# Performance work log

Hardware: AMD Instinct MI355X
Metric: run time of the kernel (lower is better)

The kernel has to match this reference:

```python
import jax, jax.numpy as jnp
import numpy as np

EMBED_DIM = 512
NUM_HEADS = 16
WIN = (8, 8)
N_TOK = WIN[0] * WIN[1]           # 64 tokens per window
HEAD_DIM = EMBED_DIM // NUM_HEADS  # 32
SCALE = HEAD_DIM ** -0.5
B_WIN = 1024                       # batch * num_windows
NUM_WINDOWS = 256                  # windows per image -> batch images = 4


def _relative_bias_index(window_size):
    wh, ww = window_size
    coords = np.stack(np.meshgrid(np.arange(wh), np.arange(ww), indexing='ij'))  # (2, wh, ww)
    flat = coords.reshape(2, -1)                                   # (2, N)
    rel = (flat[:, :, None] - flat[:, None, :]).transpose(1, 2, 0)  # (N, N, 2)
    rel[:, :, 0] += wh - 1
    rel[:, :, 1] += ww - 1
    rel[:, :, 0] *= 2 * ww - 1
    return rel.sum(-1)  # (N, N) int


def setup_inputs() -> dict:
    key = jax.random.key(0)
    ks = jax.random.split(key, 6)
    x = jax.random.normal(ks[0], (B_WIN, N_TOK, EMBED_DIM), dtype=jnp.float32)
    attention_mask = jax.random.normal(ks[1], (NUM_WINDOWS, N_TOK, N_TOK), dtype=jnp.float32)
    qkv_w = jax.random.normal(ks[2], (EMBED_DIM, 3 * EMBED_DIM), dtype=jnp.float32) * 0.02
    qkv_b = jnp.zeros((3 * EMBED_DIM,), dtype=jnp.float32)
    proj_w = jax.random.normal(ks[3], (EMBED_DIM, EMBED_DIM), dtype=jnp.float32) * 0.02
    proj_b = jnp.zeros((EMBED_DIM,), dtype=jnp.float32)
    n_bias = (2 * WIN[0] - 1) * (2 * WIN[1] - 1)  # 225
    bias_table = jax.random.normal(ks[4], (n_bias, NUM_HEADS), dtype=jnp.float32) * 0.02
    rel_index = jnp.asarray(_relative_bias_index(WIN), dtype=jnp.int32)  # (N, N)
    return {"x": x, "attention_mask": attention_mask, "qkv_w": qkv_w, "qkv_b": qkv_b,
            "proj_w": proj_w, "proj_b": proj_b, "bias_table": bias_table, "rel_index": rel_index}


def reference(x, attention_mask, qkv_w, qkv_b, proj_w, proj_b, bias_table, rel_index):
    B, N, C = x.shape
    nw = attention_mask.shape[0]
    bimg = B // nw
    qkv = x @ qkv_w + qkv_b                              # (B, N, 3C)
    # original rearrange 'b n (h d c) -> d b n h c' groups last dim as (heads, 3, head_dim)
    qkv = qkv.reshape(B, N, NUM_HEADS, 3, HEAD_DIM)
    q, k, v = qkv[..., 0, :], qkv[..., 1, :], qkv[..., 2, :]  # each (B, N, H, hd)
    attn = jnp.einsum('bqhd,bkhd->bhqk', q, k) * SCALE        # (B, H, N, N)
    bias = bias_table[rel_index].transpose(2, 0, 1)           # (H, N, N)
    attn = attn + bias[None]
    attn = attn.reshape(bimg, nw, NUM_HEADS, N, N) + attention_mask[None, :, None]
    attn = jax.nn.softmax(attn, axis=-1).reshape(B, NUM_HEADS, N, N)
    out = jnp.einsum('bhqk,bkhd->bqhd', attn, v).reshape(B, N, C)
    return out @ proj_w + proj_b
```

## Files before the change

### kernel.cpp

```cpp
#include <hip/hip_runtime.h>
#include <hip/hip_bf16.h>


typedef unsigned short u16;
typedef __bf16 bx8 __attribute__((ext_vector_type(8)));
typedef float f4_t __attribute__((ext_vector_type(4)));

#define QKV_ELEMS 33554432ull
#define SCALE 0.17677669529663687f

static __device__ __forceinline__ u16 f2b(float f) {
    return __builtin_bit_cast(u16, (__bf16)f);
}

typedef const unsigned int __attribute__((address_space(1)))* gas_t;
typedef unsigned int __attribute__((address_space(3)))* las_t;
static __device__ __forceinline__ void glds16(const void* g, void* l) {
    __builtin_amdgcn_global_load_lds((gas_t)g, (las_t)l, 16, 0, 0);
}

__global__ void cvt_k(const float* __restrict__ X, u16* __restrict__ Xb) {
    size_t i = ((size_t)blockIdx.x * 256 + threadIdx.x) * 8;
    float4 v0 = *(const float4*)(X + i);
    float4 v1 = *(const float4*)(X + i + 4);
    ushort4 p0, p1;
    p0.x = f2b(v0.x); p0.y = f2b(v0.y); p0.z = f2b(v0.z); p0.w = f2b(v0.w);
    p1.x = f2b(v1.x); p1.y = f2b(v1.y); p1.z = f2b(v1.z); p1.w = f2b(v1.w);
    *(ushort4*)(Xb + i) = p0;
    *(ushort4*)(Xb + i + 4) = p1;
}

__global__ void wt_k(const float* __restrict__ W, u16* __restrict__ Wt,
                     int K, int N) {
    int idx = blockIdx.x * 256 + threadIdx.x;
    if (idx >= N * K) return;
    int n = idx / K, k = idx - n * K;
    Wt[idx] = f2b(W[(size_t)k * N + n]);
}

__global__ void bias_k(const float* __restrict__ bias_table,
                       const int* __restrict__ rel_index,
                       float* __restrict__ bias_full) {
    int idx = blockIdx.x * 256 + threadIdx.x;
    int h = idx >> 12, rc = idx & 4095;
    bias_full[idx] = bias_table[rel_index[rc] * 16 + h];
}

template <int MODE>
__global__ __launch_bounds__(256) void gemm_k(
    const u16* __restrict__ A, const u16* __restrict__ Bt,
    const float* __restrict__ bias, void* __restrict__ Out, int K) {
    const int tid  = threadIdx.x;
    const int wave = tid >> 6, lane = tid & 63;
    const int quad = lane >> 4, l16 = lane & 15;
    const int wm = wave >> 1, wn = wave & 1;
    const int m0 = blockIdx.y * 128, n0 = blockIdx.x * 128;

    __shared__ alignas(16) char smem[17408];
    u16* a_s = (u16*)smem;
    u16* b_s = (u16*)(smem + 8192);

    const int lr = lane >> 2, lc = (lane & 3) * 8;
    const int w16 = wave * 16;

    f4_t acc[4][4];
#pragma unroll
    for (int i = 0; i < 4; ++i)
#pragma unroll
        for (int j = 0; j < 4; ++j) acc[i][j] = (f4_t){0.f, 0.f, 0.f, 0.f};

    for (int kt = 0; kt < K; kt += 32) {
        if (MODE == 0) {
            const u16* Ab = A + (size_t)m0 * K + kt;
            glds16(Ab + (size_t)(w16 + lr) * K + lc,      &a_s[w16 * 32]);
            glds16(Ab + (size_t)(w16 + 64 + lr) * K + lc, &a_s[(w16 + 64) * 32]);
        } else {
            const u16* Ab = A + (((size_t)(kt >> 5) * 1024 + (m0 >> 6)) << 11);
            glds16(Ab + ((w16 + lr) << 5) + lc,        &a_s[w16 * 32]);
            glds16(Ab + 2048 + ((w16 + lr) << 5) + lc, &a_s[(w16 + 64) * 32]);
        }
        const u16* Bb = Bt + (size_t)n0 * K + kt;
        glds16(Bb + (size_t)(w16 + lr) * K + lc,      &b_s[w16 * 32]);
        glds16(Bb + (size_t)(w16 + 64 + lr) * K + lc, &b_s[(w16 + 64) * 32]);
        __syncthreads();

        bx8 af[4], bfr[4];
#pragma unroll
        for (int mt = 0; mt < 4; ++mt)
            af[mt] = *(const bx8*)&a_s[(wm * 64 + mt * 16 + l16) * 32 + quad * 8];
#pragma unroll
        for (int nt = 0; nt < 4; ++nt)
            bfr[nt] = *(const bx8*)&b_s[(wn * 64 + nt * 16 + l16) * 32 + quad * 8];
#pragma unroll
        for (int mt = 0; mt < 4; ++mt)
#pragma unroll
            for (int nt = 0; nt < 4; ++nt)
                acc[mt][nt] = __builtin_amdgcn_mfma_f32_16x16x32_bf16(
                    af[mt], bfr[nt], acc[mt][nt], 0, 0, 0);
        __syncthreads();
    }

    float bv[4];
#pragma unroll
    for (int nt = 0; nt < 4; ++nt) bv[nt] = bias[n0 + wn * 64 + nt * 16 + l16];

    if (MODE == 0) {
        u16* c_s = (u16*)smem;
        u16* qkv = (u16*)Out;
        const int g = tid >> 6, s = tid & 63;
        const int cgb = n0 + g * 32;
        const int h = cgb / 96, rr = cgb - h * 96;
        const int which = rr >> 5;
#pragma unroll
        for (int p = 0; p < 2; ++p) {
            if (wm == p) {
#pragma unroll
                for (int mt = 0; mt < 4; ++mt)
#pragma unroll
                    for (int nt = 0; nt < 4; ++nt)
#pragma unroll
                        for (int i = 0; i < 4; ++i)
                            c_s[(mt * 16 + quad * 4 + i) * 136 +
                                wn * 64 + nt * 16 + l16] =
                                f2b(acc[mt][nt][i] + bv[nt]);
            }
            __syncthreads();
            const int w = (m0 >> 6) + p;
            u16* dst = qkv + (size_t)which * QKV_ELEMS +
                       ((size_t)((w << 4) + h) << 11);
#pragma unroll
            for (int j = 0; j < 4; ++j) {
                int idx = s + 64 * j;
                int tok = idx >> 2, d8 = (idx & 3) * 8;
                uint4 v = *(const uint4*)&c_s[tok * 136 + g * 32 + d8];
                *(uint4*)(dst + idx * 8) = v;
            }
            __syncthreads();
        }
    } else {
        float* c_sf = (float*)smem;
        float* Of = (float*)Out;
#pragma unroll
        for (int p = 0; p < 4; ++p) {
            if (wm == (p >> 1)) {
                const int mtb = (p & 1) * 2;
#pragma unroll
                for (int mt2 = 0; mt2 < 2; ++mt2)
#pragma unroll
                    for (int nt = 0; nt < 4; ++nt)
#pragma unroll
                        for (int i = 0; i < 4; ++i)
                            c_sf[(mt2 * 16 + quad * 4 + i) * 136 +
                                 wn * 64 + nt * 16 + l16] =
                                acc[mtb + mt2][nt][i] + bv[nt];
            }
            __syncthreads();
#pragma unroll
            for (int j = 0; j < 4; ++j) {
                int fl = tid + 256 * j;
                int row = fl >> 5, c4 = (fl & 31) * 4;
                float4 v = *(const float4*)&c_sf[row * 136 + c4];
                *(float4*)&Of[(size_t)(m0 + p * 32 + row) * 512 + n0 + c4] = v;
            }
            __syncthreads();
        }
    }
}

__global__ __launch_bounds__(256) void attn_k(
    const u16* __restrict__ qkv, const float* __restrict__ mask,
    const float* __restrict__ biasf, u16* __restrict__ attn_out) {
    const int bx = blockIdx.x;
    const int w = bx >> 4, h = bx & 15;
    const int wmk = w & 255;
    const int tid = threadIdx.x;
    const int wave = tid >> 6, lane = tid & 63;
    const int quad = lane >> 4, l16 = lane & 15;

    __shared__ alignas(16) u16 q_s[64 * 40];
    __shared__ alignas(16) u16 k_s[64 * 40];
    __shared__ alignas(16) u16 vT[32 * 72];
    __shared__ alignas(16) float s_s[64 * 68];
    __shared__ alignas(16) u16 p_s[64 * 72];

    const size_t base = (size_t)((w << 4) + h) * 2048;
    {
        int tok = tid >> 2, d0 = (tid & 3) * 8;
        uint4 qv = *(const uint4*)(qkv + base + tid * 8);
        *(uint4*)&q_s[tok * 40 + d0] = qv;
        uint4 kv = *(const uint4*)(qkv + QKV_ELEMS + base + tid * 8);
        *(uint4*)&k_s[tok * 40 + d0] = kv;
        uint4 vv = *(const uint4*)(qkv + 2 * QKV_ELEMS + base + tid * 8);
        const u16* pv = (const u16*)&vv;
#pragma unroll
        for (int j = 0; j < 8; ++j) vT[(d0 + j) * 72 + tok] = pv[j];
    }
    __syncthreads();

    {
        bx8 a = *(const bx8*)&q_s[(wave * 16 + l16) * 40 + quad * 8];
#pragma unroll
        for (int nt = 0; nt < 4; ++nt) {
            bx8 b = *(const bx8*)&k_s[(nt * 16 + l16) * 40 + quad * 8];
            f4_t acc = (f4_t){0.f, 0.f, 0.f, 0.f};
            acc = __builtin_amdgcn_mfma_f32_16x16x32_bf16(a, b, acc, 0, 0, 0);
#pragma unroll
            for (int i = 0; i < 4; ++i) {
                int r = wave * 16 + quad * 4 + i;
                int c = nt * 16 + l16;
                float s = acc[i] * SCALE + biasf[(h << 12) + (r << 6) + c] +
                          mask[((size_t)wmk * 64 + r) * 64 + c];
                s_s[r * 68 + c] = s;
            }
        }
    }
    __syncthreads();

    {
        int row = tid >> 2, j = (tid & 3) * 16;
        float mx = -1e30f;
#pragma unroll
        for (int cc = 0; cc < 16; ++cc) mx = fmaxf(mx, s_s[row * 68 + j + cc]);
        mx = fmaxf(mx, __shfl_xor(mx, 1));
        mx = fmaxf(mx, __shfl_xor(mx, 2));
        float e[16], sum = 0.f;
#pragma unroll
        for (int cc = 0; cc < 16; ++cc) {
            e[cc] = __expf(s_s[row * 68 + j + cc] - mx);
            sum += e[cc];
        }
        sum += __shfl_xor(sum, 1);
        sum += __shfl_xor(sum, 2);
        float inv = 1.f / sum;
#pragma unroll
        for (int cc = 0; cc < 16; ++cc) p_s[row * 72 + j + cc] = f2b(e[cc] * inv);
    }
    __syncthreads();

    {
        u16* os = (u16*)s_s;
#pragma unroll
        for (int nt = 0; nt < 2; ++nt) {
            f4_t acc = (f4_t){0.f, 0.f, 0.f, 0.f};
#pragma unroll
            for (int ks = 0; ks < 2; ++ks) {
                bx8 a = *(const bx8*)&p_s[(wave * 16 + l16) * 72 + ks * 32 + quad * 8];
                bx8 b = *(const bx8*)&vT[(nt * 16 + l16) * 72 + ks * 32 + quad * 8];
                acc = __builtin_amdgcn_mfma_f32_16x16x32_bf16(a, b, acc, 0, 0, 0);
            }
#pragma unroll
            for (int i = 0; i < 4; ++i)
                os[(wave * 16 + quad * 4 + i) * 40 + nt * 16 + l16] =
                    f2b(acc[i]);
        }
        __syncthreads();
        int tok = tid >> 2, d8 = (tid & 3) * 8;
        uint4 v = *(const uint4*)&os[tok * 40 + d8];
        *(uint4*)(attn_out + ((((size_t)h << 10) + w) << 11) + tid * 8) = v;
    }
}

extern "C" void kernel_launch(void* const* d_in, const int* in_sizes, int n_in,
                              void* d_out, int out_size, void* d_ws,
                              size_t ws_size, hipStream_t stream) {
    const float* x      = (const float*)d_in[0];
    const float* mask   = (const float*)d_in[1];
    const float* qkv_w  = (const float*)d_in[2];
    const float* qkv_b  = (const float*)d_in[3];
    const float* proj_w = (const float*)d_in[4];
    const float* proj_b = (const float*)d_in[5];
    const float* bias_t = (const float*)d_in[6];
    const int*   rel    = (const int*)d_in[7];
    float* out = (float*)d_out;

    char* ws = (char*)d_ws;
    u16* Wt1 = (u16*)ws;      ws += (size_t)1536 * 512 * 2;
    u16* Wt2 = (u16*)ws;      ws += (size_t)512 * 512 * 2;
    float* biasf = (float*)ws; ws += (size_t)16 * 64 * 64 * 4;
    u16* qkv = (u16*)ws;      ws += 3 * QKV_ELEMS * 2;
    u16* attn = (u16*)ws;     ws += QKV_ELEMS * 2;
    u16* xb = attn;

    cvt_k<<<16384, 256, 0, stream>>>(x, xb);
    wt_k<<<3072, 256, 0, stream>>>(qkv_w, Wt1, 512, 1536);
    wt_k<<<1024, 256, 0, stream>>>(proj_w, Wt2, 512, 512);
    bias_k<<<256, 256, 0, stream>>>(bias_t, rel, biasf);
    gemm_k<0><<<dim3(12, 512), 256, 0, stream>>>(xb, Wt1, qkv_b, qkv, 512);
    attn_k<<<16384, 256, 0, stream>>>(qkv, mask, biasf, attn);
    gemm_k<1><<<dim3(4, 512), 256, 0, stream>>>(attn, Wt2, proj_b, out, 512);
}
```

Baseline: 549.4 us.

## Fuse prep kernels, double-buffer GEMMs with larger tiles and swizzled LDS

Merges the four preprocessing kernels into one launch to cut launch overhead. Reworks both GEMMs into 256x128 tiles with 512 threads, double-buffered global-to-LDS staging, XOR-swizzled LDS layout, MFMA priority hints, and a grouped block-order swizzle for L2 reuse. Also pads the attention score buffer differently and adds occupancy hints. It uses more LDS per block and a fully unrolled K loop that assumes K=512.

```diff
diff --git a/kernel.cpp b/kernel.cpp
--- a/kernel.cpp
+++ b/kernel.cpp
@@ -19,49 +19,83 @@
     __builtin_amdgcn_global_load_lds((gas_t)g, (las_t)l, 16, 0, 0);
 }
 
-__global__ void cvt_k(const float* __restrict__ X, u16* __restrict__ Xb) {
-    size_t i = ((size_t)blockIdx.x * 256 + threadIdx.x) * 8;
-    float4 v0 = *(const float4*)(X + i);
-    float4 v1 = *(const float4*)(X + i + 4);
-    ushort4 p0, p1;
-    p0.x = f2b(v0.x); p0.y = f2b(v0.y); p0.z = f2b(v0.z); p0.w = f2b(v0.w);
-    p1.x = f2b(v1.x); p1.y = f2b(v1.y); p1.z = f2b(v1.z); p1.w = f2b(v1.w);
-    *(ushort4*)(Xb + i) = p0;
-    *(ushort4*)(Xb + i + 4) = p1;
-}
-
-__global__ void wt_k(const float* __restrict__ W, u16* __restrict__ Wt,
-                     int K, int N) {
-    int idx = blockIdx.x * 256 + threadIdx.x;
-    if (idx >= N * K) return;
-    int n = idx / K, k = idx - n * K;
-    Wt[idx] = f2b(W[(size_t)k * N + n]);
-}
-
-__global__ void bias_k(const float* __restrict__ bias_table,
-                       const int* __restrict__ rel_index,
-                       float* __restrict__ bias_full) {
-    int idx = blockIdx.x * 256 + threadIdx.x;
-    int h = idx >> 12, rc = idx & 4095;
-    bias_full[idx] = bias_table[rel_index[rc] * 16 + h];
+__global__ __launch_bounds__(256) void prep_k(
+    const float* __restrict__ X, u16* __restrict__ Xb,
+    const float* __restrict__ qkv_w, u16* __restrict__ Wt1,
+    const float* __restrict__ proj_w, u16* __restrict__ Wt2,
+    const float* __restrict__ bias_t, const int* __restrict__ rel,
+    float* __restrict__ biasf) {
+    const int b = blockIdx.x;
+    if (b < 16384) {
+        size_t i = ((size_t)b * 256 + threadIdx.x) * 8;
+        float4 v0 = *(const float4*)(X + i);
+        float4 v1 = *(const float4*)(X + i + 4);
+        ushort4 p0, p1;
+        p0.x = f2b(v0.x); p0.y = f2b(v0.y); p0.z = f2b(v0.z); p0.w = f2b(v0.w);
+        p1.x = f2b(v1.x); p1.y = f2b(v1.y); p1.z = f2b(v1.z); p1.w = f2b(v1.w);
+        *(ushort4*)(Xb + i) = p0;
+        *(ushort4*)(Xb + i + 4) = p1;
+    } else if (b < 16384 + 3072) {
+        int idx = (b - 16384) * 256 + threadIdx.x;
+        int n = idx >> 9, k = idx & 511;
+        Wt1[idx] = f2b(qkv_w[(size_t)k * 1536 + n]);
+    } else if (b < 16384 + 4096) {
+        int idx = (b - 16384 - 3072) * 256 + threadIdx.x;
+        int n = idx >> 9, k = idx & 511;
+        Wt2[idx] = f2b(proj_w[(size_t)k * 512 + n]);
+    } else {
+        int idx = (b - 16384 - 4096) * 256 + threadIdx.x;
+        int h = idx >> 12, rc = idx & 4095;
+        biasf[idx] = bias_t[rel[rc] * 16 + h];
+    }
 }
 
 template <int MODE>
-__global__ __launch_bounds__(256) void gemm_k(
+__global__ __launch_bounds__(512, 4) void gemm_k(
     const u16* __restrict__ A, const u16* __restrict__ Bt,
-    const float* __restrict__ bias, void* __restrict__ Out, int K) {
-    const int tid  = threadIdx.x;
+    const float* __restrict__ bias, void* __restrict__ Out) {
+    extern __shared__ __align__(16) char smem[];
+    const int tid = threadIdx.x;
     const int wave = tid >> 6, lane = tid & 63;
-    const int quad = lane >> 4, l16 = lane & 15;
+    const int l16 = lane & 15, quad = lane >> 4;
     const int wm = wave >> 1, wn = wave & 1;
-    const int m0 = blockIdx.y * 128, n0 = blockIdx.x * 128;
-
-    __shared__ alignas(16) char smem[17408];
-    u16* a_s = (u16*)smem;
-    u16* b_s = (u16*)(smem + 8192);
-
-    const int lr = lane >> 2, lc = (lane & 3) * 8;
-    const int w16 = wave * 16;
+
+    const int NT_COL = (MODE == 0) ? 12 : 4;
+    const int NWG = (MODE == 0) ? 3072 : 1024;
+    const int bid = blockIdx.x;
+    const int swz = (bid & 7) * (NWG >> 3) + (bid >> 3);
+    const int m0 = (swz / NT_COL) << 8;
+    const int n0 = (swz % NT_COL) << 7;
+
+    const int lr = lane >> 2, lc = lane & 3;
+    const int swzc = (lc ^ ((lr >> 1) & 3)) * 8;
+    const int stoff = wave * 1024;
+
+    const u16* Asrc0;
+    const u16* Asrc1;
+    if (MODE == 0) {
+        Asrc0 = A + (size_t)(m0 + wave * 16 + lr) * 512 + swzc;
+        Asrc1 = Asrc0 + (size_t)128 * 512;
+    } else {
+        const int r0 = m0 + wave * 16 + lr, r1 = r0 + 128;
+        Asrc0 = A + (size_t)(r0 >> 6) * 2048 + (r0 & 63) * 32 + swzc;
+        Asrc1 = A + (size_t)(r1 >> 6) * 2048 + (r1 & 63) * 32 + swzc;
+    }
+    const u16* Bsrc0 = Bt + (size_t)(n0 + wave * 16 + lr) * 512 + swzc;
+
+    auto STAGE = [&](int T) {
+        char* base = smem + (T & 1) * 24576;
+        if (MODE == 0) {
+            glds16(Asrc0 + (size_t)T * 32, base + stoff);
+            glds16(Asrc1 + (size_t)T * 32, base + 8192 + stoff);
+        } else {
+            glds16(Asrc0 + (size_t)T * 2097152, base + stoff);
+            glds16(Asrc1 + (size_t)T * 2097152, base + 8192 + stoff);
+        }
+        glds16(Bsrc0 + (size_t)T * 32, base + 16384 + stoff);
+    };
+
+    const int foff = l16 * 64 + ((quad ^ ((l16 >> 1) & 3)) * 16);
 
     f4_t acc[4][4];
 #pragma unroll
@@ -69,34 +103,28 @@
 #pragma unroll
         for (int j = 0; j < 4; ++j) acc[i][j] = (f4_t){0.f, 0.f, 0.f, 0.f};
 
-    for (int kt = 0; kt < K; kt += 32) {
-        if (MODE == 0) {
-            const u16* Ab = A + (size_t)m0 * K + kt;
-            glds16(Ab + (size_t)(w16 + lr) * K + lc,      &a_s[w16 * 32]);
-            glds16(Ab + (size_t)(w16 + 64 + lr) * K + lc, &a_s[(w16 + 64) * 32]);
-        } else {
-            const u16* Ab = A + (((size_t)(kt >> 5) * 1024 + (m0 >> 6)) << 11);
-            glds16(Ab + ((w16 + lr) << 5) + lc,        &a_s[w16 * 32]);
-            glds16(Ab + 2048 + ((w16 + lr) << 5) + lc, &a_s[(w16 + 64) * 32]);
-        }
-        const u16* Bb = Bt + (size_t)n0 * K + kt;
-        glds16(Bb + (size_t)(w16 + lr) * K + lc,      &b_s[w16 * 32]);
-        glds16(Bb + (size_t)(w16 + 64 + lr) * K + lc, &b_s[(w16 + 64) * 32]);
-        __syncthreads();
-
-        bx8 af[4], bfr[4];
-#pragma unroll
-        for (int mt = 0; mt < 4; ++mt)
-            af[mt] = *(const bx8*)&a_s[(wm * 64 + mt * 16 + l16) * 32 + quad * 8];
-#pragma unroll
-        for (int nt = 0; nt < 4; ++nt)
-            bfr[nt] = *(const bx8*)&b_s[(wn * 64 + nt * 16 + l16) * 32 + quad * 8];
+    STAGE(0);
+    __syncthreads();
+
+    #pragma unroll
+    for (int T = 0; T < 16; ++T) {
+        if (T < 15) STAGE(T + 1);
+        const char* sb = smem + (T & 1) * 24576;
+        const char* aT = sb + wm * 4096 + foff;
+        const char* bT = sb + 16384 + wn * 4096 + foff;
+        bx8 af[4], bf[4];
+#pragma unroll
+        for (int i = 0; i < 4; ++i) af[i] = *(const bx8*)(aT + i * 1024);
+#pragma unroll
+        for (int i = 0; i < 4; ++i) bf[i] = *(const bx8*)(bT + i * 1024);
+        __builtin_amdgcn_s_setprio(1);
 #pragma unroll
         for (int mt = 0; mt < 4; ++mt)
 #pragma unroll
             for (int nt = 0; nt < 4; ++nt)
                 acc[mt][nt] = __builtin_amdgcn_mfma_f32_16x16x32_bf16(
-                    af[mt], bfr[nt], acc[mt][nt], 0, 0, 0);
+                    af[mt], bf[nt], acc[mt][nt], 0, 0, 0);
+        __builtin_amdgcn_s_setprio(0);
         __syncthreads();
     }
 
@@ -106,13 +134,10 @@
 
     if (MODE == 0) {
         u16* c_s = (u16*)smem;
-        u16* qkv = (u16*)Out;
-        const int g = tid >> 6, s = tid & 63;
-        const int cgb = n0 + g * 32;
-        const int h = cgb / 96, rr = cgb - h * 96;
-        const int which = rr >> 5;
-#pragma unroll
-        for (int p = 0; p < 2; ++p) {
+        u16* qkvp = (u16*)Out;
+        const int wwin = m0 >> 6;
+#pragma unroll
+        for (int p = 0; p < 4; ++p) {
             if (wm == p) {
 #pragma unroll
                 for (int mt = 0; mt < 4; ++mt)
@@ -120,20 +145,23 @@
                     for (int nt = 0; nt < 4; ++nt)
 #pragma unroll
                         for (int i = 0; i < 4; ++i)
-                            c_s[(mt * 16 + quad * 4 + i) * 136 +
+                            c_s[(mt * 16 + quad * 4 + i) * 132 +
                                 wn * 64 + nt * 16 + l16] =
                                 f2b(acc[mt][nt][i] + bv[nt]);
             }
             __syncthreads();
-            const int w = (m0 >> 6) + p;
-            u16* dst = qkv + (size_t)which * QKV_ELEMS +
-                       ((size_t)((w << 4) + h) << 11);
-#pragma unroll
-            for (int j = 0; j < 4; ++j) {
-                int idx = s + 64 * j;
+#pragma unroll
+            for (int j = 0; j < 2; ++j) {
+                int flat = tid + 512 * j;
+                int g2 = flat >> 8, idx = flat & 255;
                 int tok = idx >> 2, d8 = (idx & 3) * 8;
-                uint4 v = *(const uint4*)&c_s[tok * 136 + g * 32 + d8];
-                *(uint4*)(dst + idx * 8) = v;
+                int cg = n0 + g2 * 32;
+                int hh = cg / 96;
+                int which = (cg - hh * 96) >> 5;
+                uint4 v = *(const uint4*)&c_s[tok * 132 + g2 * 32 + d8];
+                *(uint4*)(qkvp + (size_t)which * QKV_ELEMS +
+                          (size_t)hh * 2048 +
+                          (size_t)(wwin + p) * 32768 + tok * 32 + d8) = v;
             }
             __syncthreads();
         }
@@ -142,32 +170,31 @@
         float* Of = (float*)Out;
 #pragma unroll
         for (int p = 0; p < 4; ++p) {
-            if (wm == (p >> 1)) {
-                const int mtb = (p & 1) * 2;
-#pragma unroll
-                for (int mt2 = 0; mt2 < 2; ++mt2)
+            if (wm == p) {
+#pragma unroll
+                for (int mt = 0; mt < 4; ++mt)
 #pragma unroll
                     for (int nt = 0; nt < 4; ++nt)
 #pragma unroll
                         for (int i = 0; i < 4; ++i)
-                            c_sf[(mt2 * 16 + quad * 4 + i) * 136 +
+                            c_sf[(mt * 16 + quad * 4 + i) * 132 +
                                  wn * 64 + nt * 16 + l16] =
-                                acc[mtb + mt2][nt][i] + bv[nt];
+                                acc[mt][nt][i] + bv[nt];
             }
             __syncthreads();
 #pragma unroll
             for (int j = 0; j < 4; ++j) {
-                int fl = tid + 256 * j;
-                int row = fl >> 5, c4 = (fl & 31) * 4;
-                float4 v = *(const float4*)&c_sf[row * 136 + c4];
-                *(float4*)&Of[(size_t)(m0 + p * 32 + row) * 512 + n0 + c4] = v;
+                int flat = tid + 512 * j;
+                int r = flat >> 5, c4 = (flat & 31) * 4;
+                float4 v = *(const float4*)&c_sf[r * 132 + c4];
+                *(float4*)&Of[(size_t)(m0 + p * 64 + r) * 512 + n0 + c4] = v;
             }
             __syncthreads();
         }
     }
 }
 
-__global__ __launch_bounds__(256) void attn_k(
+__global__ __launch_bounds__(256, 4) void attn_k(
     const u16* __restrict__ qkv, const float* __restrict__ mask,
     const float* __restrict__ biasf, u16* __restrict__ attn_out) {
     const int bx = blockIdx.x;
@@ -180,7 +207,7 @@
     __shared__ alignas(16) u16 q_s[64 * 40];
     __shared__ alignas(16) u16 k_s[64 * 40];
     __shared__ alignas(16) u16 vT[32 * 72];
-    __shared__ alignas(16) float s_s[64 * 68];
+    __shared__ alignas(16) float s_s[64 * 65];
     __shared__ alignas(16) u16 p_s[64 * 72];
 
     const size_t base = (size_t)((w << 4) + h) * 2048;
@@ -210,7 +237,7 @@
                 int c = nt * 16 + l16;
                 float s = acc[i] * SCALE + biasf[(h << 12) + (r << 6) + c] +
                           mask[((size_t)wmk * 64 + r) * 64 + c];
-                s_s[r * 68 + c] = s;
+                s_s[r * 65 + c] = s;
             }
         }
     }
@@ -220,13 +247,13 @@
         int row = tid >> 2, j = (tid & 3) * 16;
         float mx = -1e30f;
 #pragma unroll
-        for (int cc = 0; cc < 16; ++cc) mx = fmaxf(mx, s_s[row * 68 + j + cc]);
+        for (int cc = 0; cc < 16; ++cc) mx = fmaxf(mx, s_s[row * 65 + j + cc]);
         mx = fmaxf(mx, __shfl_xor(mx, 1));
         mx = fmaxf(mx, __shfl_xor(mx, 2));
         float e[16], sum = 0.f;
 #pragma unroll
         for (int cc = 0; cc < 16; ++cc) {
-            e[cc] = __expf(s_s[row * 68 + j + cc] - mx);
+            e[cc] = __expf(s_s[row * 65 + j + cc] - mx);
             sum += e[cc];
         }
         sum += __shfl_xor(sum, 1);
@@ -281,11 +308,9 @@
     u16* attn = (u16*)ws;     ws += QKV_ELEMS * 2;
     u16* xb = attn;
 
-    cvt_k<<<16384, 256, 0, stream>>>(x, xb);
-    wt_k<<<3072, 256, 0, stream>>>(qkv_w, Wt1, 512, 1536);
-    wt_k<<<1024, 256, 0, stream>>>(proj_w, Wt2, 512, 512);
-    bias_k<<<256, 256, 0, stream>>>(bias_t, rel, biasf);
-    gemm_k<0><<<dim3(12, 512), 256, 0, stream>>>(xb, Wt1, qkv_b, qkv, 512);
+    prep_k<<<20736, 256, 0, stream>>>(x, xb, qkv_w, Wt1, proj_w, Wt2,
+                                      bias_t, rel, biasf);
+    gemm_k<0><<<3072, 512, 49152, stream>>>(xb, Wt1, qkv_b, qkv);
     attn_k<<<16384, 256, 0, stream>>>(qkv, mask, biasf, attn);
-    gemm_k<1><<<dim3(4, 512), 256, 0, stream>>>(attn, Wt2, proj_b, out, 512);
-}
+    gemm_k<1><<<1024, 512, 49152, stream>>>(attn, Wt2, proj_b, out);
+}
```

After: 488.7 us. 1.12x faster.
